# Kernel tuning notes

Measured on AMD Instinct MI355X. Metric: run time of the kernel, lower is better.

The kernel has to match this reference:

```python
import jax, jax.numpy as jnp
import numpy as np

NUM_CODES = 8192
CODE_DEPTH = 64
D_MODEL = 1024
NUM_LEVELS = 1


def setup_inputs() -> dict:
    key = jax.random.key(0)
    k1, k2, k3, k4 = jax.random.split(key, 4)
    x = jax.random.normal(k1, (8, 2048, D_MODEL), dtype=jnp.float32)
    # nn.Linear(d_model, code_depth): weight [code_depth, d_model], bias [code_depth]
    W_down = jax.random.normal(k2, (CODE_DEPTH, D_MODEL), dtype=jnp.float32) * 0.02
    b_down = jnp.zeros((CODE_DEPTH,), dtype=jnp.float32)
    # codebook = torch.randn(num_levels, num_codes, code_depth)
    codebook = jax.random.normal(k3, (NUM_LEVELS, NUM_CODES, CODE_DEPTH), dtype=jnp.float32)
    return {"x": x, "W_down": W_down, "b_down": b_down, "codebook": codebook}


def reference(x, W_down, b_down, codebook):
    # downsample: Linear(d_model -> code_depth), level 0
    soft = jnp.einsum("bsd,cd->bsc", x, W_down) + b_down  # [B,S,C]
    book = codebook[0]  # [K,C]
    # cdist(x, book).argmin == argmin of squared distances (sqrt is monotone)
    x2 = jnp.sum(soft * soft, axis=-1, keepdims=True)      # [B,S,1]
    c2 = jnp.sum(book * book, axis=-1)                     # [K]
    xc = jnp.einsum("bsc,kc->bsk", soft, book)             # [B,S,K]
    sq_dist = x2 - 2.0 * xc + c2                           # [B,S,K]
    code_indices = jnp.argmin(sq_dist, axis=-1)            # [B,S] int
    hard = book[code_indices]                              # [B,S,C]
    # training-mode losses (mse_loss = mean over all elements)
    commitment_loss = jnp.mean((jax.lax.stop_gradient(hard) - soft) ** 2)
    embedding_loss = jnp.mean((hard - jax.lax.stop_gradient(soft)) ** 2)
    # straight-through estimator
    hard_ste = soft + jax.lax.stop_gradient(hard - soft)
    return (soft, code_indices, hard_ste, commitment_loss, embedding_loss)
```

## Files before the change

kernel.cpp:

```cpp
#include <hip/hip_runtime.h>

#define M_TOT   16384
#define DM      1024
#define CD      64
#define NCODES  8192
#define NCHUNK  16
#define CPC     (NCODES / NCHUNK)

#define SOFT_OFF  0
#define IDX_OFF   1048576
#define HARD_OFF  1064960
#define LOSS_OFF  2113536

__global__ __launch_bounds__(256) void compute_c2(const float* __restrict__ book,
                                                  float* __restrict__ c2) {
    const int k = blockIdx.x * 256 + threadIdx.x;
    const float4* p = (const float4*)(book + (size_t)k * CD);
    float s = 0.0f;
#pragma unroll
    for (int q = 0; q < CD / 4; ++q) {
        const float4 v = p[q];
        s = fmaf(v.x, v.x, s);
        s = fmaf(v.y, v.y, s);
        s = fmaf(v.z, v.z, s);
        s = fmaf(v.w, v.w, s);
    }
    c2[k] = s;
}

__global__ __launch_bounds__(256) void soft_gemm_k(const float* __restrict__ x,
                                                   const float* __restrict__ W,
                                                   const float* __restrict__ bias,
                                                   float* __restrict__ dst,
                                                   int kchunk) {
    __shared__ float xt[32][68];
    __shared__ float wt[32][68];

    const int tid = threadIdx.x;
    const int r0  = blockIdx.x * 64;
    const int k0base = blockIdx.y * kchunk;
    const int cg  = tid & 15;
    const int rg  = tid >> 4;

    float acc[4][4] = {};

    for (int k0 = k0base; k0 < k0base + kchunk; k0 += 32) {
#pragma unroll
        for (int i = 0; i < 2; ++i) {
            const int f   = tid + i * 256;
            const int row = f >> 3;
            const int kq  = (f & 7) * 4;
            const float4 v = *(const float4*)(x + (size_t)(r0 + row) * DM + k0 + kq);
            xt[kq + 0][row] = v.x; xt[kq + 1][row] = v.y;
            xt[kq + 2][row] = v.z; xt[kq + 3][row] = v.w;
            const float4 w = *(const float4*)(W + (size_t)row * DM + k0 + kq);
            wt[kq + 0][row] = w.x; wt[kq + 1][row] = w.y;
            wt[kq + 2][row] = w.z; wt[kq + 3][row] = w.w;
        }
        __syncthreads();
#pragma unroll 8
        for (int kk = 0; kk < 32; ++kk) {
            const float4 xv = *(const float4*)&xt[kk][rg * 4];
            const float4 wv = *(const float4*)&wt[kk][cg * 4];
            const float xa[4] = {xv.x, xv.y, xv.z, xv.w};
            const float wa[4] = {wv.x, wv.y, wv.z, wv.w};
#pragma unroll
            for (int r = 0; r < 4; ++r)
#pragma unroll
                for (int q = 0; q < 4; ++q)
                    acc[r][q] = fmaf(xa[r], wa[q], acc[r][q]);
        }
        __syncthreads();
    }

    float4 bb = make_float4(0.f, 0.f, 0.f, 0.f);
    if (bias) bb = *(const float4*)(bias + cg * 4);
    float* base = dst + (size_t)blockIdx.y * M_TOT * CD;
#pragma unroll
    for (int r = 0; r < 4; ++r) {
        float4 o;
        o.x = acc[r][0] + bb.x; o.y = acc[r][1] + bb.y;
        o.z = acc[r][2] + bb.z; o.w = acc[r][3] + bb.w;
        *(float4*)(base + (size_t)(r0 + rg * 4 + r) * CD + cg * 4) = o;
    }
}

__global__ __launch_bounds__(256) void soft_reduce(const float* __restrict__ partial,
                                                   const float* __restrict__ bias,
                                                   float* __restrict__ out_soft,
                                                   int nsplit) {
    const int i = blockIdx.x * 256 + threadIdx.x;
    const float4* p = (const float4*)partial;
    float4 s = p[i];
    for (int j = 1; j < nsplit; ++j) {
        const float4 v = p[(size_t)j * (M_TOT * CD / 4) + i];
        s.x += v.x; s.y += v.y; s.z += v.z; s.w += v.w;
    }
    const float4 bb = ((const float4*)bias)[i & 15];
    s.x += bb.x; s.y += bb.y; s.z += bb.z; s.w += bb.w;
    ((float4*)out_soft)[i] = s;
}

__global__ __launch_bounds__(256) void dist_argmin2(const float* __restrict__ soft,
                                                    const float* __restrict__ book,
                                                    const float* __restrict__ c2,
                                                    float* __restrict__ cand_d,
                                                    int* __restrict__ cand_i) {
    const int row   = blockIdx.x * 256 + threadIdx.x;
    const int kbase = blockIdx.y * CPC;

    float4 s4[16];
    const float4* sp = (const float4*)(soft + (size_t)row * CD);
#pragma unroll
    for (int q = 0; q < 16; ++q) s4[q] = sp[q];

    float mind = 3.4e38f;
    int   mini = kbase;
    const float4* bp = (const float4*)(book + (size_t)kbase * CD);

    for (int kk = 0; kk < CPC; kk += 4) {
        const float4* b0 = bp + (size_t)(kk + 0) * 16;
        const float4* b1 = bp + (size_t)(kk + 1) * 16;
        const float4* b2 = bp + (size_t)(kk + 2) * 16;
        const float4* b3 = bp + (size_t)(kk + 3) * 16;
        float a0 = 0.f, a1 = 0.f, a2 = 0.f, a3 = 0.f;
#pragma unroll
        for (int q = 0; q < 16; ++q) {
            const float4 sv = s4[q];
            const float4 v0 = b0[q];
            a0 = fmaf(sv.x, v0.x, a0); a0 = fmaf(sv.y, v0.y, a0);
            a0 = fmaf(sv.z, v0.z, a0); a0 = fmaf(sv.w, v0.w, a0);
            const float4 v1 = b1[q];
            a1 = fmaf(sv.x, v1.x, a1); a1 = fmaf(sv.y, v1.y, a1);
            a1 = fmaf(sv.z, v1.z, a1); a1 = fmaf(sv.w, v1.w, a1);
            const float4 v2 = b2[q];
            a2 = fmaf(sv.x, v2.x, a2); a2 = fmaf(sv.y, v2.y, a2);
            a2 = fmaf(sv.z, v2.z, a2); a2 = fmaf(sv.w, v2.w, a2);
            const float4 v3 = b3[q];
            a3 = fmaf(sv.x, v3.x, a3); a3 = fmaf(sv.y, v3.y, a3);
            a3 = fmaf(sv.z, v3.z, a3); a3 = fmaf(sv.w, v3.w, a3);
        }
        const int k = kbase + kk;
        const float d0 = fmaf(-2.f, a0, c2[k + 0]);
        const float d1 = fmaf(-2.f, a1, c2[k + 1]);
        const float d2 = fmaf(-2.f, a2, c2[k + 2]);
        const float d3 = fmaf(-2.f, a3, c2[k + 3]);
        if (d0 < mind) { mind = d0; mini = k + 0; }
        if (d1 < mind) { mind = d1; mini = k + 1; }
        if (d2 < mind) { mind = d2; mini = k + 2; }
        if (d3 < mind) { mind = d3; mini = k + 3; }
    }

    cand_d[blockIdx.y * M_TOT + row] = mind;
    cand_i[blockIdx.y * M_TOT + row] = mini;
}

__global__ __launch_bounds__(256) void finalize(const float* __restrict__ book,
                                                const float* __restrict__ cand_d,
                                                const int* __restrict__ cand_i,
                                                float* __restrict__ out) {
    __shared__ float rd[256];
    __shared__ int   ri[256];
    __shared__ int   ksels[16];
    __shared__ float red[256];

    const int tid  = threadIdx.x;
    const int rloc = tid >> 4;
    const int g    = tid & 15;
    const int row  = blockIdx.x * 16 + rloc;

    rd[tid] = cand_d[(size_t)g * M_TOT + row];
    ri[tid] = cand_i[(size_t)g * M_TOT + row];
    __syncthreads();

    if (g == 0) {
        float bd = rd[rloc * 16];
        int   bi = ri[rloc * 16];
#pragma unroll
        for (int j = 1; j < 16; ++j) {
            const float dd = rd[rloc * 16 + j];
            if (dd < bd) { bd = dd; bi = ri[rloc * 16 + j]; }
        }
        ksels[rloc] = bi;
        out[IDX_OFF + row] = (float)bi;
    }
    __syncthreads();

    const int k  = ksels[rloc];
    const int dq = g * 4;

    const float4 h = *(const float4*)(book + (size_t)k * CD + dq);
    const float4 s = *(const float4*)(out + SOFT_OFF + (size_t)row * CD + dq);

    const float dx = h.x - s.x, dy = h.y - s.y, dz = h.z - s.z, dw = h.w - s.w;
    float4 ste;
    ste.x = s.x + dx; ste.y = s.y + dy; ste.z = s.z + dz; ste.w = s.w + dw;
    *(float4*)(out + HARD_OFF + (size_t)row * CD + dq) = ste;

    red[tid] = dx * dx + dy * dy + dz * dz + dw * dw;
    __syncthreads();
#pragma unroll
    for (int sh = 128; sh > 0; sh >>= 1) {
        if (tid < sh) red[tid] += red[tid + sh];
        __syncthreads();
    }
    if (tid == 0) {
        const float v = red[0] * (1.0f / (float)(M_TOT * CD));
        atomicAdd(out + LOSS_OFF, v);
        atomicAdd(out + LOSS_OFF + 1, v);
    }
}

extern "C" void kernel_launch(void* const* d_in, const int* in_sizes, int n_in,
                              void* d_out, int out_size, void* d_ws, size_t ws_size,
                              hipStream_t stream) {
    const float* x    = (const float*)d_in[0];
    const float* W    = (const float*)d_in[1];
    const float* bias = (const float*)d_in[2];
    const float* book = (const float*)d_in[3];
    float* out = (float*)d_out;

    float* ws     = (float*)d_ws;
    float* c2     = ws;
    float* cand_d = ws + NCODES;
    int*   cand_i = (int*)(cand_d + NCHUNK * M_TOT);
    float* partial = (float*)(cand_i + NCHUNK * M_TOT);

    const size_t base_floats = NCODES + (size_t)2 * NCHUNK * M_TOT;
    int splitk = 4;
    if (ws_size < (base_floats + (size_t)splitk * M_TOT * CD) * sizeof(float))
        splitk = 1;

    compute_c2<<<NCODES / 256, 256, 0, stream>>>(book, c2);

    if (splitk == 4) {
        soft_gemm_k<<<dim3(M_TOT / 64, 4), 256, 0, stream>>>(x, W, nullptr, partial, DM / 4);
        soft_reduce<<<M_TOT * CD / 4 / 256, 256, 0, stream>>>(partial, bias, out + SOFT_OFF, 4);
    } else {
        soft_gemm_k<<<dim3(M_TOT / 64, 1), 256, 0, stream>>>(x, W, bias, out + SOFT_OFF, DM);
    }

    dist_argmin2<<<dim3(M_TOT / 256, NCHUNK), 256, 0, stream>>>(out + SOFT_OFF, book, c2,
                                                                cand_d, cand_i);
    hipMemsetAsync(out + LOSS_OFF, 0, 2 * sizeof(float), stream);
    finalize<<<M_TOT / 16, 256, 0, stream>>>(book, cand_d, cand_i, out);
}
```

Measured before the change: 531.1 us.

## Fuse split-K soft GEMM reduction in-block and retile distance argmin over codes

```diff
diff --git a/kernel.cpp b/kernel.cpp
--- a/kernel.cpp
+++ b/kernel.cpp
@@ -6,6 +6,7 @@
 #define NCODES  8192
 #define NCHUNK  16
 #define CPC     (NCODES / NCHUNK)
+#define CTILE   16
 
 #define SOFT_OFF  0
 #define IDX_OFF   1048576
@@ -28,40 +29,40 @@
     c2[k] = s;
 }
 
-__global__ __launch_bounds__(256) void soft_gemm_k(const float* __restrict__ x,
-                                                   const float* __restrict__ W,
-                                                   const float* __restrict__ bias,
-                                                   float* __restrict__ dst,
-                                                   int kchunk) {
-    __shared__ float xt[32][68];
-    __shared__ float wt[32][68];
+__global__ __launch_bounds__(1024, 1) void soft_fused(const float* __restrict__ x,
+                                                      const float* __restrict__ W,
+                                                      const float* __restrict__ bias,
+                                                      float* __restrict__ out_soft) {
+    __shared__ float smem[8704];
+    float (*xt)[16][68] = (float (*)[16][68])smem;
+    float (*wt)[16][68] = (float (*)[16][68])(smem + 4352);
+    float (*pb)[32][65] = (float (*)[32][65])smem;
 
     const int tid = threadIdx.x;
+    const int kg  = tid >> 8;
+    const int t   = tid & 255;
     const int r0  = blockIdx.x * 64;
-    const int k0base = blockIdx.y * kchunk;
-    const int cg  = tid & 15;
-    const int rg  = tid >> 4;
+    const int rg  = t >> 4;
+    const int cg  = t & 15;
 
     float acc[4][4] = {};
 
-    for (int k0 = k0base; k0 < k0base + kchunk; k0 += 32) {
-#pragma unroll
-        for (int i = 0; i < 2; ++i) {
-            const int f   = tid + i * 256;
-            const int row = f >> 3;
-            const int kq  = (f & 7) * 4;
+    for (int k0 = kg * 256; k0 < kg * 256 + 256; k0 += 16) {
+        {
+            const int row = t >> 2;
+            const int kq  = (t & 3) * 4;
             const float4 v = *(const float4*)(x + (size_t)(r0 + row) * DM + k0 + kq);
-            xt[kq + 0][row] = v.x; xt[kq + 1][row] = v.y;
-            xt[kq + 2][row] = v.z; xt[kq + 3][row] = v.w;
+            xt[kg][kq + 0][row] = v.x; xt[kg][kq + 1][row] = v.y;
+            xt[kg][kq + 2][row] = v.z; xt[kg][kq + 3][row] = v.w;
             const float4 w = *(const float4*)(W + (size_t)row * DM + k0 + kq);
-            wt[kq + 0][row] = w.x; wt[kq + 1][row] = w.y;
-            wt[kq + 2][row] = w.z; wt[kq + 3][row] = w.w;
-        }
-        __syncthreads();
-#pragma unroll 8
-        for (int kk = 0; kk < 32; ++kk) {
-            const float4 xv = *(const float4*)&xt[kk][rg * 4];
-            const float4 wv = *(const float4*)&wt[kk][cg * 4];
+            wt[kg][kq + 0][row] = w.x; wt[kg][kq + 1][row] = w.y;
+            wt[kg][kq + 2][row] = w.z; wt[kg][kq + 3][row] = w.w;
+        }
+        __syncthreads();
+#pragma unroll
+        for (int kk = 0; kk < 16; ++kk) {
+            const float4 xv = *(const float4*)&xt[kg][kk][rg * 4];
+            const float4 wv = *(const float4*)&wt[kg][kk][cg * 4];
             const float xa[4] = {xv.x, xv.y, xv.z, xv.w};
             const float wa[4] = {wv.x, wv.y, wv.z, wv.w};
 #pragma unroll
@@ -73,82 +74,65 @@
         __syncthreads();
     }
 
-    float4 bb = make_float4(0.f, 0.f, 0.f, 0.f);
-    if (bias) bb = *(const float4*)(bias + cg * 4);
-    float* base = dst + (size_t)blockIdx.y * M_TOT * CD;
-#pragma unroll
-    for (int r = 0; r < 4; ++r) {
-        float4 o;
-        o.x = acc[r][0] + bb.x; o.y = acc[r][1] + bb.y;
-        o.z = acc[r][2] + bb.z; o.w = acc[r][3] + bb.w;
-        *(float4*)(base + (size_t)(r0 + rg * 4 + r) * CD + cg * 4) = o;
-    }
-}
-
-__global__ __launch_bounds__(256) void soft_reduce(const float* __restrict__ partial,
-                                                   const float* __restrict__ bias,
-                                                   float* __restrict__ out_soft,
-                                                   int nsplit) {
-    const int i = blockIdx.x * 256 + threadIdx.x;
-    const float4* p = (const float4*)partial;
-    float4 s = p[i];
-    for (int j = 1; j < nsplit; ++j) {
-        const float4 v = p[(size_t)j * (M_TOT * CD / 4) + i];
-        s.x += v.x; s.y += v.y; s.z += v.z; s.w += v.w;
-    }
-    const float4 bb = ((const float4*)bias)[i & 15];
-    s.x += bb.x; s.y += bb.y; s.z += bb.z; s.w += bb.w;
-    ((float4*)out_soft)[i] = s;
-}
-
-__global__ __launch_bounds__(256) void dist_argmin2(const float* __restrict__ soft,
-                                                    const float* __restrict__ book,
-                                                    const float* __restrict__ c2,
-                                                    float* __restrict__ cand_d,
-                                                    int* __restrict__ cand_i) {
+#pragma unroll
+    for (int half = 0; half < 2; ++half) {
+        if ((rg >> 3) == half) {
+#pragma unroll
+            for (int r = 0; r < 4; ++r)
+                *(float4*)&pb[kg][(rg & 7) * 4 + r][cg * 4] =
+                    make_float4(acc[r][0], acc[r][1], acc[r][2], acc[r][3]);
+        }
+        __syncthreads();
+        if (tid < 512) {
+            const int row = tid >> 4;
+            const int qd  = tid & 15;
+            float4 s = *(const float4*)&pb[0][row][qd * 4];
+#pragma unroll
+            for (int g = 1; g < 4; ++g) {
+                const float4 v = *(const float4*)&pb[g][row][qd * 4];
+                s.x += v.x; s.y += v.y; s.z += v.z; s.w += v.w;
+            }
+            const float4 bb = *(const float4*)(bias + qd * 4);
+            s.x += bb.x; s.y += bb.y; s.z += bb.z; s.w += bb.w;
+            *(float4*)(out_soft + (size_t)(r0 + half * 32 + row) * CD + qd * 4) = s;
+        }
+        __syncthreads();
+    }
+}
+
+__global__ __launch_bounds__(256, 4) void dist_argmin3(const float* __restrict__ soft,
+                                                       const float* __restrict__ book,
+                                                       const float* __restrict__ c2,
+                                                       float* __restrict__ cand_d,
+                                                       int* __restrict__ cand_i) {
     const int row   = blockIdx.x * 256 + threadIdx.x;
     const int kbase = blockIdx.y * CPC;
-
-    float4 s4[16];
     const float4* sp = (const float4*)(soft + (size_t)row * CD);
-#pragma unroll
-    for (int q = 0; q < 16; ++q) s4[q] = sp[q];
 
     float mind = 3.4e38f;
     int   mini = kbase;
-    const float4* bp = (const float4*)(book + (size_t)kbase * CD);
-
-    for (int kk = 0; kk < CPC; kk += 4) {
-        const float4* b0 = bp + (size_t)(kk + 0) * 16;
-        const float4* b1 = bp + (size_t)(kk + 1) * 16;
-        const float4* b2 = bp + (size_t)(kk + 2) * 16;
-        const float4* b3 = bp + (size_t)(kk + 3) * 16;
-        float a0 = 0.f, a1 = 0.f, a2 = 0.f, a3 = 0.f;
+
+    for (int kt = 0; kt < CPC; kt += CTILE) {
+        const float4* bp = (const float4*)(book + (size_t)(kbase + kt) * CD);
+        float acc[CTILE] = {};
 #pragma unroll
         for (int q = 0; q < 16; ++q) {
-            const float4 sv = s4[q];
-            const float4 v0 = b0[q];
-            a0 = fmaf(sv.x, v0.x, a0); a0 = fmaf(sv.y, v0.y, a0);
-            a0 = fmaf(sv.z, v0.z, a0); a0 = fmaf(sv.w, v0.w, a0);
-            const float4 v1 = b1[q];
-            a1 = fmaf(sv.x, v1.x, a1); a1 = fmaf(sv.y, v1.y, a1);
-            a1 = fmaf(sv.z, v1.z, a1); a1 = fmaf(sv.w, v1.w, a1);
-            const float4 v2 = b2[q];
-            a2 = fmaf(sv.x, v2.x, a2); a2 = fmaf(sv.y, v2.y, a2);
-            a2 = fmaf(sv.z, v2.z, a2); a2 = fmaf(sv.w, v2.w, a2);
-            const float4 v3 = b3[q];
-            a3 = fmaf(sv.x, v3.x, a3); a3 = fmaf(sv.y, v3.y, a3);
-            a3 = fmaf(sv.z, v3.z, a3); a3 = fmaf(sv.w, v3.w, a3);
-        }
-        const int k = kbase + kk;
-        const float d0 = fmaf(-2.f, a0, c2[k + 0]);
-        const float d1 = fmaf(-2.f, a1, c2[k + 1]);
-        const float d2 = fmaf(-2.f, a2, c2[k + 2]);
-        const float d3 = fmaf(-2.f, a3, c2[k + 3]);
-        if (d0 < mind) { mind = d0; mini = k + 0; }
-        if (d1 < mind) { mind = d1; mini = k + 1; }
-        if (d2 < mind) { mind = d2; mini = k + 2; }
-        if (d3 < mind) { mind = d3; mini = k + 3; }
+            const float4 sv = sp[q];
+#pragma unroll
+            for (int c = 0; c < CTILE; ++c) {
+                const float4 bv = bp[(size_t)c * 16 + q];
+                acc[c] = fmaf(sv.x, bv.x, acc[c]);
+                acc[c] = fmaf(sv.y, bv.y, acc[c]);
+                acc[c] = fmaf(sv.z, bv.z, acc[c]);
+                acc[c] = fmaf(sv.w, bv.w, acc[c]);
+            }
+        }
+        const int kk0 = kbase + kt;
+#pragma unroll
+        for (int c = 0; c < CTILE; ++c) {
+            const float dd = fmaf(-2.f, acc[c], c2[kk0 + c]);
+            if (dd < mind) { mind = dd; mini = kk0 + c; }
+        }
     }
 
     cand_d[blockIdx.y * M_TOT + row] = mind;
@@ -224,23 +208,10 @@
     float* c2     = ws;
     float* cand_d = ws + NCODES;
     int*   cand_i = (int*)(cand_d + NCHUNK * M_TOT);
-    float* partial = (float*)(cand_i + NCHUNK * M_TOT);
-
-    const size_t base_floats = NCODES + (size_t)2 * NCHUNK * M_TOT;
-    int splitk = 4;
-    if (ws_size < (base_floats + (size_t)splitk * M_TOT * CD) * sizeof(float))
-        splitk = 1;
 
     compute_c2<<<NCODES / 256, 256, 0, stream>>>(book, c2);
-
-    if (splitk == 4) {
-        soft_gemm_k<<<dim3(M_TOT / 64, 4), 256, 0, stream>>>(x, W, nullptr, partial, DM / 4);
-        soft_reduce<<<M_TOT * CD / 4 / 256, 256, 0, stream>>>(partial, bias, out + SOFT_OFF, 4);
-    } else {
-        soft_gemm_k<<<dim3(M_TOT / 64, 1), 256, 0, stream>>>(x, W, bias, out + SOFT_OFF, DM);
-    }
-
-    dist_argmin2<<<dim3(M_TOT / 256, NCHUNK), 256, 0, stream>>>(out + SOFT_OFF, book, c2,
+    soft_fused<<<M_TOT / 64, 1024, 0, stream>>>(x, W, bias, out + SOFT_OFF);
+    dist_argmin3<<<dim3(M_TOT / 256, NCHUNK), 256, 0, stream>>>(out + SOFT_OFF, book, c2,
                                                                 cand_d, cand_i);
     hipMemsetAsync(out + LOSS_OFF, 0, 2 * sizeof(float), stream);
     finalize<<<M_TOT / 16, 256, 0, stream>>>(book, cand_d, cand_i, out);
```

Result: slower. 563.6 us (+6.1%).
